# Performance work log

Hardware: AMD Instinct MI355X
Metric: run time of the kernel (lower is better)

Reference implementation:

```python
import jax, jax.numpy as jnp
import numpy as np

HEADS = 8
DIM_HEAD = 80
BATCH_SIZE = 2  # cfg batch (module init kwarg)


def setup_inputs() -> dict:
    key = jax.random.key(0)
    ks = jax.random.split(key, 6)
    F, S, D = 16, 1024, 640  # frames*batch, latent HW, query_dim
    hidden_states = jax.random.normal(ks[0], (F, S, D), jnp.float32)
    Wq = jax.random.normal(ks[1], (D, D), jnp.float32) * 0.02
    Wk = jax.random.normal(ks[2], (D, D), jnp.float32) * 0.02
    Wv = jax.random.normal(ks[3], (D, D), jnp.float32) * 0.02
    Wo = jax.random.normal(ks[4], (D, D), jnp.float32) * 0.02
    bo = jax.random.normal(ks[5], (D,), jnp.float32) * 0.02
    return {"hidden_states": hidden_states, "Wq": Wq, "Wk": Wk, "Wv": Wv, "Wo": Wo, "bo": bo}


def reference(hidden_states, Wq, Wk, Wv, Wo, bo):
    F, S, D = hidden_states.shape
    h, d = HEADS, DIM_HEAD
    scale = d ** -0.5

    q = hidden_states @ Wq  # [F, S, D]
    k = hidden_states @ Wk
    v = hidden_states @ Wv

    # cross-frame trick: replace every frame's K/V with the FIRST frame of its batch group
    vl = 1 if F < BATCH_SIZE else F // BATCH_SIZE  # video_length
    g = F // vl  # batch groups
    k = jnp.broadcast_to(k.reshape(g, vl, S, D)[:, :1], (g, vl, S, D)).reshape(F, S, D)
    v = jnp.broadcast_to(v.reshape(g, vl, S, D)[:, :1], (g, vl, S, D)).reshape(F, S, D)

    def to_heads(t):  # [F, S, h*d] -> [F*h, S, d]
        return t.reshape(F, S, h, d).transpose(0, 2, 1, 3).reshape(F * h, S, d)

    qh, kh, vh = to_heads(q), to_heads(k), to_heads(v)

    scores = jnp.einsum('bid,bjd->bij', qh, kh) * scale  # [F*h, S, S]
    probs = jax.nn.softmax(scores, axis=-1)
    out = jnp.einsum('bij,bjd->bid', probs, vh)  # [F*h, S, d]

    out = out.reshape(F, h, S, d).transpose(0, 2, 1, 3).reshape(F, S, h * d)
    return out @ Wo + bo
```

## Files before the change

kernel.cpp:

```cpp
#include <hip/hip_runtime.h>
#include <hip/hip_bf16.h>

typedef unsigned short u16;
typedef unsigned int u32;
typedef __attribute__((ext_vector_type(8))) short bf16x8;
typedef __attribute__((ext_vector_type(4))) float f32x4;

#define D640 640

__device__ __forceinline__ float b2f(u16 u) {
  union { u32 i; float f; } x; x.i = ((u32)u) << 16; return x.f;
}
__device__ __forceinline__ u16 f2b(float f) {
  union { __hip_bfloat16 h; u16 u; } c; c.h = __float2bfloat16(f); return c.u;
}
__device__ __forceinline__ u32 pack2(float a, float b) {
  union { __hip_bfloat162 h; u32 u; } c;
  c.h.x = __float2bfloat16(a); c.h.y = __float2bfloat16(b); return c.u;
}
__device__ __forceinline__ bf16x8 pack8(f32x4 lo, f32x4 hi) {
  bf16x8 r;
  r[0] = (short)f2b(lo[0]); r[1] = (short)f2b(lo[1]);
  r[2] = (short)f2b(lo[2]); r[3] = (short)f2b(lo[3]);
  r[4] = (short)f2b(hi[0]); r[5] = (short)f2b(hi[1]);
  r[6] = (short)f2b(hi[2]); r[7] = (short)f2b(hi[3]);
  return r;
}

__global__ void detect_dtype(const u16* __restrict__ hs, u32* __restrict__ flag) {
  __shared__ u32 cnt;
  if (threadIdx.x == 0) cnt = 0;
  __syncthreads();
  int plaus = 0;
#pragma unroll
  for (int i = 0; i < 16; ++i) {
    u16 u = hs[(threadIdx.x * 16 + i) * 2];
    u32 e = (u >> 7) & 0xFF;
    if ((e >= 0x70 && e <= 0x8F) || (u & 0x7FFF) == 0) plaus++;
  }
  atomicAdd(&cnt, (u32)plaus);
  __syncthreads();
  if (threadIdx.x == 0) *flag = (cnt < 2048) ? 1u : 0u;
}

__global__ __launch_bounds__(256) void transpose_w(
    const void* __restrict__ w0, const void* __restrict__ w1,
    const void* __restrict__ w2, const void* __restrict__ w3,
    u16* __restrict__ out, const u32* __restrict__ flag)
{
  __shared__ u16 t[32][33];
  const bool isF32 = (*flag != 0);
  const void* src = blockIdx.z == 0 ? w0 : blockIdx.z == 1 ? w1 : blockIdx.z == 2 ? w2 : w3;
  u16* dst = out + (size_t)blockIdx.z * 409600;
  int tx = threadIdx.x, ty = threadIdx.y;
  int x = blockIdx.x * 32 + tx;
  int y = blockIdx.y * 32 + ty;
  if (isF32) {
    const float* s = (const float*)src;
#pragma unroll
    for (int j = 0; j < 32; j += 8) t[ty + j][tx] = f2b(s[(y + j) * D640 + x]);
  } else {
    const u16* s = (const u16*)src;
#pragma unroll
    for (int j = 0; j < 32; j += 8) t[ty + j][tx] = s[(y + j) * D640 + x];
  }
  __syncthreads();
  int x2 = blockIdx.y * 32 + tx;
  int y2 = blockIdx.x * 32 + ty;
#pragma unroll
  for (int j = 0; j < 32; j += 8) dst[(y2 + j) * D640 + x2] = t[tx][ty + j];
}

__device__ __forceinline__ void gemm_body(
    const void* __restrict__ Av, const u16* __restrict__ BT, void* __restrict__ Cv,
    float scale, bool isF32, int aRow0, int cMode, int bx, int by)
{
  __shared__ __align__(16) u16 Asub[128 * 32];
  __shared__ __align__(16) u16 Bsub[128 * 32];
  const bool aF32 = isF32;
  const int tid = threadIdx.x;
  const int lane = tid & 63, w = tid >> 6;
  const int wr = w >> 1, wc = w & 1;
  const int l15 = lane & 15, g = lane >> 4;
  const int rowBase = bx * 128;
  const int colBase = by * 128;

  const int r0 = tid >> 2, r1 = r0 + 64, gc = tid & 3;
  const int ls0 = r0 * 4 + (gc ^ ((r0 >> 1) & 3));
  const int ls1 = r1 * 4 + (gc ^ ((r1 >> 1) & 3));
  const size_t aIdx0 = (size_t)(aRow0 + rowBase + r0) * D640 + gc * 8;
  const size_t aIdx1 = (size_t)(aRow0 + rowBase + r1) * D640 + gc * 8;
  const u16* Bg0 = BT + (colBase + r0) * D640 + gc * 8;
  const u16* Bg1 = BT + (colBase + r1) * D640 + gc * 8;

  int aoff[4], boff[4];
#pragma unroll
  for (int f = 0; f < 4; ++f) {
    int R = wr * 64 + f * 16 + l15;
    aoff[f] = (R * 4 + (g ^ ((R >> 1) & 3))) * 8;
    int Cc = wc * 64 + f * 16 + l15;
    boff[f] = (Cc * 4 + (g ^ ((Cc >> 1) & 3))) * 8;
  }

  f32x4 acc[4][4];
#pragma unroll
  for (int i = 0; i < 4; ++i)
#pragma unroll
    for (int j = 0; j < 4; ++j) acc[i][j] = (f32x4){0.f, 0.f, 0.f, 0.f};

  bf16x8 ra0, ra1, rb0, rb1;
  if (aF32) {
    const float* Af = (const float*)Av;
    ra0 = pack8(*(const f32x4*)(Af + aIdx0), *(const f32x4*)(Af + aIdx0 + 4));
    ra1 = pack8(*(const f32x4*)(Af + aIdx1), *(const f32x4*)(Af + aIdx1 + 4));
  } else {
    const u16* Ab = (const u16*)Av;
    ra0 = *(const bf16x8*)(Ab + aIdx0);
    ra1 = *(const bf16x8*)(Ab + aIdx1);
  }
  rb0 = *(const bf16x8*)Bg0;
  rb1 = *(const bf16x8*)Bg1;

  for (int kt = 0; kt < 20; ++kt) {
    __syncthreads();
    *(bf16x8*)&Asub[ls0 * 8] = ra0;
    *(bf16x8*)&Asub[ls1 * 8] = ra1;
    *(bf16x8*)&Bsub[ls0 * 8] = rb0;
    *(bf16x8*)&Bsub[ls1 * 8] = rb1;
    __syncthreads();
    if (kt < 19) {
      const int k1 = (kt + 1) * 32;
      if (aF32) {
        const float* Af = (const float*)Av;
        ra0 = pack8(*(const f32x4*)(Af + aIdx0 + k1), *(const f32x4*)(Af + aIdx0 + k1 + 4));
        ra1 = pack8(*(const f32x4*)(Af + aIdx1 + k1), *(const f32x4*)(Af + aIdx1 + k1 + 4));
      } else {
        const u16* Ab = (const u16*)Av;
        ra0 = *(const bf16x8*)(Ab + aIdx0 + k1);
        ra1 = *(const bf16x8*)(Ab + aIdx1 + k1);
      }
      rb0 = *(const bf16x8*)(Bg0 + k1);
      rb1 = *(const bf16x8*)(Bg1 + k1);
    }
    bf16x8 a[4], b[4];
#pragma unroll
    for (int f = 0; f < 4; ++f) a[f] = *(const bf16x8*)&Asub[aoff[f]];
#pragma unroll
    for (int f = 0; f < 4; ++f) b[f] = *(const bf16x8*)&Bsub[boff[f]];
    __builtin_amdgcn_s_setprio(1);
#pragma unroll
    for (int i = 0; i < 4; ++i)
#pragma unroll
      for (int j = 0; j < 4; ++j)
        acc[i][j] = __builtin_amdgcn_mfma_f32_16x16x32_bf16(a[i], b[j], acc[i][j], 0, 0, 0);
    __builtin_amdgcn_s_setprio(0);
  }

#pragma unroll
  for (int j = 0; j < 4; ++j) {
    int col = colBase + wc * 64 + j * 16 + l15;
#pragma unroll
    for (int i = 0; i < 4; ++i) {
      int row = rowBase + wr * 64 + i * 16 + g * 4;
#pragma unroll
      for (int r = 0; r < 4; ++r) {
        float v = acc[i][j][r] * scale;
        if (cMode == 2) ((u16*)Cv)[(size_t)col * 1024 + (row + r)] = f2b(v);
        else            ((u16*)Cv)[(size_t)(row + r) * D640 + col] = f2b(v);
      }
    }
  }
}

__global__ __launch_bounds__(256) void gemm_kv(
    const void* __restrict__ hs, const u16* __restrict__ WTk, const u16* __restrict__ WTv,
    u16* __restrict__ Kb, u16* __restrict__ Vb, const u32* __restrict__ flag)
{
  const int z = blockIdx.z;
  const bool isK = (z < 2);
  const int grp = z & 1;
  const u16* bt = isK ? WTk : WTv;
  void* cv = isK ? (void*)(Kb + (size_t)grp * 1024 * 640)
                 : (void*)(Vb + (size_t)grp * 655360);
  gemm_body(hs, bt, cv, 1.f, (*flag != 0), grp * 8192, isK ? 0 : 2,
            blockIdx.x, blockIdx.y);
}

__global__ __launch_bounds__(256) void gemm2(
    const void* __restrict__ Av, const u16* __restrict__ BT, void* __restrict__ Cv,
    float scale, const void* __restrict__ bias, const u32* __restrict__ flag,
    int aF32mode, int cF32mode)
{
  __shared__ __align__(16) u16 Asub[128 * 32];
  __shared__ __align__(16) u16 Bsub[160 * 32];
  const bool isF32 = (*flag != 0);
  const bool aF32 = aF32mode && isF32;
  const bool cF32 = cF32mode && isF32;
  const int tid = threadIdx.x;
  const int lane = tid & 63, w = tid >> 6;
  const int wr = w >> 1, wc = w & 1;
  const int l15 = lane & 15, g = lane >> 4;
  const int rowBase = blockIdx.x * 128;
  const int colBase = blockIdx.y * 160;

  const int ar0 = tid >> 2, ar1 = ar0 + 64, gc = tid & 3;
  const int als0 = ar0 * 4 + (gc ^ ((ar0 >> 1) & 3));
  const int als1 = ar1 * 4 + (gc ^ ((ar1 >> 1) & 3));
  const size_t aIdx0 = (size_t)(rowBase + ar0) * D640 + gc * 8;
  const size_t aIdx1 = (size_t)(rowBase + ar1) * D640 + gc * 8;
  const bool hasB3 = (tid < 128);
  const int br0 = ar0, br1 = ar1, br2 = hasB3 ? (128 + (tid >> 2)) : 0;
  const int bls0 = als0, bls1 = als1;
  const int bls2 = br2 * 4 + (gc ^ ((br2 >> 1) & 3));
  const u16* Bg0 = BT + (colBase + br0) * D640 + gc * 8;
  const u16* Bg1 = BT + (colBase + br1) * D640 + gc * 8;
  const u16* Bg2 = BT + (colBase + br2) * D640 + gc * 8;

  int aoff[4], boff[5];
#pragma unroll
  for (int f = 0; f < 4; ++f) {
    int R = wr * 64 + f * 16 + l15;
    aoff[f] = (R * 4 + (g ^ ((R >> 1) & 3))) * 8;
  }
#pragma unroll
  for (int j = 0; j < 5; ++j) {
    int Cc = wc * 80 + j * 16 + l15;
    boff[j] = (Cc * 4 + (g ^ ((Cc >> 1) & 3))) * 8;
  }

  f32x4 acc[4][5];
#pragma unroll
  for (int i = 0; i < 4; ++i)
#pragma unroll
    for (int j = 0; j < 5; ++j) acc[i][j] = (f32x4){0.f, 0.f, 0.f, 0.f};

  bf16x8 ra0, ra1, rb0, rb1, rb2;
  if (aF32) {
    const float* Af = (const float*)Av;
    ra0 = pack8(*(const f32x4*)(Af + aIdx0), *(const f32x4*)(Af + aIdx0 + 4));
    ra1 = pack8(*(const f32x4*)(Af + aIdx1), *(const f32x4*)(Af + aIdx1 + 4));
  } else {
    const u16* Ab = (const u16*)Av;
    ra0 = *(const bf16x8*)(Ab + aIdx0);
    ra1 = *(const bf16x8*)(Ab + aIdx1);
  }
  rb0 = *(const bf16x8*)Bg0;
  rb1 = *(const bf16x8*)Bg1;
  rb2 = hasB3 ? *(const bf16x8*)Bg2 : (bf16x8){0,0,0,0,0,0,0,0};

  for (int kt = 0; kt < 20; ++kt) {
    __syncthreads();
    *(bf16x8*)&Asub[als0 * 8] = ra0;
    *(bf16x8*)&Asub[als1 * 8] = ra1;
    *(bf16x8*)&Bsub[bls0 * 8] = rb0;
    *(bf16x8*)&Bsub[bls1 * 8] = rb1;
    if (hasB3) *(bf16x8*)&Bsub[bls2 * 8] = rb2;
    __syncthreads();
    if (kt < 19) {
      const int k1 = (kt + 1) * 32;
      if (aF32) {
        const float* Af = (const float*)Av;
        ra0 = pack8(*(const f32x4*)(Af + aIdx0 + k1), *(const f32x4*)(Af + aIdx0 + k1 + 4));
        ra1 = pack8(*(const f32x4*)(Af + aIdx1 + k1), *(const f32x4*)(Af + aIdx1 + k1 + 4));
      } else {
        const u16* Ab = (const u16*)Av;
        ra0 = *(const bf16x8*)(Ab + aIdx0 + k1);
        ra1 = *(const bf16x8*)(Ab + aIdx1 + k1);
      }
      rb0 = *(const bf16x8*)(Bg0 + k1);
      rb1 = *(const bf16x8*)(Bg1 + k1);
      if (hasB3) rb2 = *(const bf16x8*)(Bg2 + k1);
    }
    bf16x8 a[4], b[5];
#pragma unroll
    for (int f = 0; f < 4; ++f) a[f] = *(const bf16x8*)&Asub[aoff[f]];
#pragma unroll
    for (int j = 0; j < 5; ++j) b[j] = *(const bf16x8*)&Bsub[boff[j]];
    __builtin_amdgcn_s_setprio(1);
#pragma unroll
    for (int i = 0; i < 4; ++i)
#pragma unroll
      for (int j = 0; j < 5; ++j)
        acc[i][j] = __builtin_amdgcn_mfma_f32_16x16x32_bf16(a[i], b[j], acc[i][j], 0, 0, 0);
    __builtin_amdgcn_s_setprio(0);
  }

#pragma unroll
  for (int j = 0; j < 5; ++j) {
    int col = colBase + wc * 80 + j * 16 + l15;
    float bb = 0.f;
    if (bias) bb = cF32 ? ((const float*)bias)[col] : b2f(((const u16*)bias)[col]);
#pragma unroll
    for (int i = 0; i < 4; ++i) {
      int row = rowBase + wr * 64 + i * 16 + g * 4;
#pragma unroll
      for (int r = 0; r < 4; ++r) {
        float v = acc[i][j][r] * scale + bb;
        if (cF32) ((float*)Cv)[(size_t)(row + r) * D640 + col] = v;
        else      ((u16*)Cv)[(size_t)(row + r) * D640 + col] = f2b(v);
      }
    }
  }
}

__global__ __launch_bounds__(256, 3) void attn_kernel(
    const u16* __restrict__ Q, const u16* __restrict__ K2,
    const u16* __restrict__ VT, u16* __restrict__ AO)
{
  __shared__ __align__(16) u16 Klds[64 * 104];
  __shared__ __align__(16) u16 Vlds[80 * 72];
  __shared__ __align__(16) u16 Plds[4][32 * 72];

  const int tid = threadIdx.x, lane = tid & 63, w = tid >> 6;
  const int l15 = lane & 15, g = lane >> 4;
  const int qc = blockIdx.x, bh = blockIdx.y;
  const int f = bh >> 3, h = bh & 7;
  const int grp = f >> 3;
  u16* Pw = &Plds[w][0];

  const u16* Qp = Q + (size_t)(f * 1024 + qc * 128 + w * 32) * D640 + h * 80;
  const u16* Kp = K2 + (size_t)(grp * 1024) * D640 + h * 80;
  const u16* Vp = VT + (size_t)(grp * 8 + h) * 80 * 1024;

  if (tid < 128) {
    const bf16x8 z8 = {0, 0, 0, 0, 0, 0, 0, 0};
    *(bf16x8*)&Klds[(tid >> 1) * 104 + 80 + (tid & 1) * 8] = z8;
  }

  bf16x8 qreg[2][3];
#pragma unroll
  for (int qb = 0; qb < 2; ++qb)
#pragma unroll
    for (int dc = 0; dc < 3; ++dc) {
      int dd = dc * 32 + g * 8;
      if (dd < 80) qreg[qb][dc] = *(const bf16x8*)(Qp + (l15 + 16 * qb) * D640 + dd);
      else         qreg[qb][dc] = (bf16x8){0, 0, 0, 0, 0, 0, 0, 0};
    }

  f32x4 acc[2][5];
#pragma unroll
  for (int qb = 0; qb < 2; ++qb)
#pragma unroll
    for (int db = 0; db < 5; ++db) acc[qb][db] = (f32x4){0.f, 0.f, 0.f, 0.f};
  float mreg[2] = {-1e30f, -1e30f};
  float lrow[2] = {0.f, 0.f};

  const u16* gsrc[5];
  u16* ldst[5];
  int step[5];
#pragma unroll
  for (int i = 0; i < 5; ++i) {
    int c = tid + i * 256;
    if (c < 640) {
      int row = c / 10, cc = c - row * 10;
      gsrc[i] = Kp + row * D640 + cc * 8;
      ldst[i] = &Klds[row * 104 + cc * 8];
      step[i] = 64 * D640;
    } else {
      int c2 = c - 640, d = c2 >> 3, cc = c2 & 7;
      gsrc[i] = Vp + d * 1024 + cc * 8;
      ldst[i] = &Vlds[d * 72 + cc * 8];
      step[i] = 64;
    }
  }

  bf16x8 pre[5];
#pragma unroll
  for (int i = 0; i < 5; ++i) pre[i] = *(const bf16x8*)gsrc[i];

  for (int it = 0; it < 16; ++it) {
    __syncthreads();
#pragma unroll
    for (int i = 0; i < 5; ++i) *(bf16x8*)ldst[i] = pre[i];
    __syncthreads();
    if (it < 15) {
#pragma unroll
      for (int i = 0; i < 5; ++i) pre[i] = *(const bf16x8*)(gsrc[i] + (it + 1) * step[i]);
    }

    f32x4 st[4][2];
#pragma unroll
    for (int kb = 0; kb < 4; ++kb)
#pragma unroll
      for (int qb = 0; qb < 2; ++qb) st[kb][qb] = (f32x4){0.f, 0.f, 0.f, 0.f};
    __builtin_amdgcn_s_setprio(1);
#pragma unroll
    for (int dc = 0; dc < 3; ++dc)
#pragma unroll
      for (int kb = 0; kb < 4; ++kb) {
        bf16x8 ka = *(const bf16x8*)&Klds[(kb * 16 + l15) * 104 + dc * 32 + g * 8];
        st[kb][0] = __builtin_amdgcn_mfma_f32_16x16x32_bf16(ka, qreg[0][dc], st[kb][0], 0, 0, 0);
        st[kb][1] = __builtin_amdgcn_mfma_f32_16x16x32_bf16(ka, qreg[1][dc], st[kb][1], 0, 0, 0);
      }
    __builtin_amdgcn_s_setprio(0);

    float mt[2];
#pragma unroll
    for (int qb = 0; qb < 2; ++qb) {
      float m01 = fmaxf(fmaxf(st[0][qb][0], st[0][qb][1]), fmaxf(st[0][qb][2], st[0][qb][3]));
      float m23 = fmaxf(fmaxf(st[1][qb][0], st[1][qb][1]), fmaxf(st[1][qb][2], st[1][qb][3]));
      float m45 = fmaxf(fmaxf(st[2][qb][0], st[2][qb][1]), fmaxf(st[2][qb][2], st[2][qb][3]));
      float m67 = fmaxf(fmaxf(st[3][qb][0], st[3][qb][1]), fmaxf(st[3][qb][2], st[3][qb][3]));
      float m = fmaxf(fmaxf(m01, m23), fmaxf(m45, m67));
      m = fmaxf(m, __shfl_xor(m, 16, 64));
      m = fmaxf(m, __shfl_xor(m, 32, 64));
      mt[qb] = m;
    }

    if (__any((mt[0] > mreg[0] + 8.f) || (mt[1] > mreg[1] + 8.f))) {
#pragma unroll
      for (int qb = 0; qb < 2; ++qb) {
        float mn = fmaxf(mreg[qb], mt[qb]);
        float scl = exp2f(mreg[qb] - mn);
        mreg[qb] = mn;
        lrow[qb] *= scl;
        float s_[4];
#pragma unroll
        for (int r = 0; r < 4; ++r)
          s_[r] = __shfl(scl, (lane & 48) | (g * 4 + r), 64);
#pragma unroll
        for (int db = 0; db < 5; ++db)
#pragma unroll
          for (int r = 0; r < 4; ++r) acc[qb][db][r] *= s_[r];
      }
    }

#pragma unroll
    for (int qb = 0; qb < 2; ++qb) {
      float sum = 0.f;
#pragma unroll
      for (int kb = 0; kb < 4; ++kb) {
        float p0 = exp2f(st[kb][qb][0] - mreg[qb]);
        float p1 = exp2f(st[kb][qb][1] - mreg[qb]);
        float p2 = exp2f(st[kb][qb][2] - mreg[qb]);
        float p3 = exp2f(st[kb][qb][3] - mreg[qb]);
        sum += (p0 + p1) + (p2 + p3);
        uint2 pk;
        pk.x = pack2(p0, p1);
        pk.y = pack2(p2, p3);
        *(uint2*)&Pw[(l15 + 16 * qb) * 72 + kb * 16 + g * 4] = pk;
      }
      sum += __shfl_xor(sum, 16, 64);
      sum += __shfl_xor(sum, 32, 64);
      lrow[qb] += sum;
    }

    __builtin_amdgcn_s_setprio(1);
#pragma unroll
    for (int kc = 0; kc < 2; ++kc) {
      bf16x8 pa0 = *(const bf16x8*)&Pw[(l15) * 72 + kc * 32 + g * 8];
      bf16x8 pa1 = *(const bf16x8*)&Pw[(l15 + 16) * 72 + kc * 32 + g * 8];
#pragma unroll
      for (int db = 0; db < 5; ++db) {
        bf16x8 bv = *(const bf16x8*)&Vlds[(db * 16 + l15) * 72 + kc * 32 + g * 8];
        acc[0][db] = __builtin_amdgcn_mfma_f32_16x16x32_bf16(pa0, bv, acc[0][db], 0, 0, 0);
        acc[1][db] = __builtin_amdgcn_mfma_f32_16x16x32_bf16(pa1, bv, acc[1][db], 0, 0, 0);
      }
    }
    __builtin_amdgcn_s_setprio(0);
  }

  u16* Op = AO + (size_t)(f * 1024 + qc * 128 + w * 32) * D640 + h * 80;
#pragma unroll
  for (int qb = 0; qb < 2; ++qb) {
    float i_[4];
#pragma unroll
    for (int r = 0; r < 4; ++r)
      i_[r] = 1.f / __shfl(lrow[qb], (lane & 48) | (g * 4 + r), 64);
#pragma unroll
    for (int db = 0; db < 5; ++db)
#pragma unroll
      for (int r = 0; r < 4; ++r)
        Op[(qb * 16 + g * 4 + r) * D640 + db * 16 + l15] = f2b(acc[qb][db][r] * i_[r]);
  }
}

extern "C" void kernel_launch(void* const* d_in, const int* in_sizes, int n_in,
                              void* d_out, int out_size, void* d_ws, size_t ws_size,
                              hipStream_t stream) {
  (void)in_sizes; (void)n_in; (void)out_size; (void)ws_size;
  const void* hs = d_in[0];
  const void* wq = d_in[1];
  const void* wk = d_in[2];
  const void* wv = d_in[3];
  const void* wo = d_in[4];
  const void* bo = d_in[5];
  u16* ws = (u16*)d_ws;

  u16* WT  = ws;
  u16* Qb  = ws + 1638400;
  u16* Kb  = Qb + 10485760;
  u16* Vb  = Kb + 1310720;
  u16* AOb = Vb + 1310720;
  u32* flag = (u32*)(AOb + 10485760);

  const float QSCALE = 0.11180339887498949f * 1.44269504088896340f;

  detect_dtype<<<1, 256, 0, stream>>>((const u16*)hs, flag);

  transpose_w<<<dim3(20, 20, 4), dim3(32, 8), 0, stream>>>(wq, wk, wv, wo, WT, flag);

  gemm2<<<dim3(128, 4), 256, 0, stream>>>(hs, WT, Qb, QSCALE, nullptr, flag, 1, 0);
  gemm_kv<<<dim3(8, 5, 4), 256, 0, stream>>>(hs, WT + 409600, WT + 819200, Kb, Vb, flag);

  attn_kernel<<<dim3(8, 128), 256, 0, stream>>>(Qb, Kb, Vb, AOb);

  gemm2<<<dim3(128, 4), 256, 0, stream>>>(AOb, WT + 1228800, d_out, 1.f, bo, flag, 0, 1);
}
```

Baseline: 169.8 us.

## Keep softmax probabilities in registers by permuting V^T key layout

```diff
diff --git a/kernel.cpp b/kernel.cpp
--- a/kernel.cpp
+++ b/kernel.cpp
@@ -165,8 +165,14 @@
 #pragma unroll
       for (int r = 0; r < 4; ++r) {
         float v = acc[i][j][r] * scale;
-        if (cMode == 2) ((u16*)Cv)[(size_t)col * 1024 + (row + r)] = f2b(v);
-        else            ((u16*)Cv)[(size_t)(row + r) * D640 + col] = f2b(v);
+        if (cMode == 2) {
+          int rw = row + r;
+          int rl = rw & 63;
+          int slot = (rl & 32) | ((rl & 12) << 1) | (((rl >> 4) & 1) << 2) | (rl & 3);
+          ((u16*)Cv)[(size_t)col * 1024 + (rw & ~63) + slot] = f2b(v);
+        } else {
+          ((u16*)Cv)[(size_t)(row + r) * D640 + col] = f2b(v);
+        }
       }
     }
   }
@@ -309,14 +315,12 @@
 {
   __shared__ __align__(16) u16 Klds[64 * 104];
   __shared__ __align__(16) u16 Vlds[80 * 72];
-  __shared__ __align__(16) u16 Plds[4][32 * 72];
 
   const int tid = threadIdx.x, lane = tid & 63, w = tid >> 6;
   const int l15 = lane & 15, g = lane >> 4;
   const int qc = blockIdx.x, bh = blockIdx.y;
   const int f = bh >> 3, h = bh & 7;
   const int grp = f >> 3;
-  u16* Pw = &Plds[w][0];
 
   const u16* Qp = Q + (size_t)(f * 1024 + qc * 128 + w * 32) * D640 + h * 80;
   const u16* Kp = K2 + (size_t)(grp * 1024) * D640 + h * 80;
@@ -425,9 +429,11 @@
       }
     }
 
+    bf16x8 pa[2][2];
 #pragma unroll
     for (int qb = 0; qb < 2; ++qb) {
       float sum = 0.f;
+      u32 wlo[4], whi[4];
 #pragma unroll
       for (int kb = 0; kb < 4; ++kb) {
         float p0 = exp2f(st[kb][qb][0] - mreg[qb]);
@@ -435,26 +441,31 @@
         float p2 = exp2f(st[kb][qb][2] - mreg[qb]);
         float p3 = exp2f(st[kb][qb][3] - mreg[qb]);
         sum += (p0 + p1) + (p2 + p3);
-        uint2 pk;
-        pk.x = pack2(p0, p1);
-        pk.y = pack2(p2, p3);
-        *(uint2*)&Pw[(l15 + 16 * qb) * 72 + kb * 16 + g * 4] = pk;
+        wlo[kb] = pack2(p0, p1);
+        whi[kb] = pack2(p2, p3);
       }
       sum += __shfl_xor(sum, 16, 64);
       sum += __shfl_xor(sum, 32, 64);
       lrow[qb] += sum;
+#pragma unroll
+      for (int kc = 0; kc < 2; ++kc) {
+        union { u32 u[4]; bf16x8 v; } cvt;
+        cvt.u[0] = wlo[2 * kc];
+        cvt.u[1] = whi[2 * kc];
+        cvt.u[2] = wlo[2 * kc + 1];
+        cvt.u[3] = whi[2 * kc + 1];
+        pa[qb][kc] = cvt.v;
+      }
     }
 
     __builtin_amdgcn_s_setprio(1);
 #pragma unroll
     for (int kc = 0; kc < 2; ++kc) {
-      bf16x8 pa0 = *(const bf16x8*)&Pw[(l15) * 72 + kc * 32 + g * 8];
-      bf16x8 pa1 = *(const bf16x8*)&Pw[(l15 + 16) * 72 + kc * 32 + g * 8];
 #pragma unroll
       for (int db = 0; db < 5; ++db) {
         bf16x8 bv = *(const bf16x8*)&Vlds[(db * 16 + l15) * 72 + kc * 32 + g * 8];
-        acc[0][db] = __builtin_amdgcn_mfma_f32_16x16x32_bf16(pa0, bv, acc[0][db], 0, 0, 0);
-        acc[1][db] = __builtin_amdgcn_mfma_f32_16x16x32_bf16(pa1, bv, acc[1][db], 0, 0, 0);
+        acc[0][db] = __builtin_amdgcn_mfma_f32_16x16x32_bf16(pa[0][kc], bv, acc[0][db], 0, 0, 0);
+        acc[1][db] = __builtin_amdgcn_mfma_f32_16x16x32_bf16(pa[1][kc], bv, acc[1][db], 0, 0, 0);
       }
     }
     __builtin_amdgcn_s_setprio(0);
```

Result: no change. 169.6 us (-0.1%).
